# Kernel tuning notes

Measured on AMD Instinct MI355X. Metric: run time of the kernel, lower is better.

The kernel has to match this reference:

```python
import jax, jax.numpy as jnp
import numpy as np

NUM_USERS = 4096
NUM_ITEMS = 4096
NUM_CLASSES = 5
INPUT_DIM = 64
H0 = 64   # hidden[0]
H1 = 32   # hidden[1]
BU = 2048
BV = 2048


def setup_inputs() -> dict:
    key = jax.random.key(0)
    ks = jax.random.split(key, 9)
    ridx = jax.random.randint(ks[0], (NUM_USERS, NUM_ITEMS), 0, NUM_CLASSES * 10)
    ratings = (jnp.arange(NUM_CLASSES)[:, None, None] == ridx[None]).astype(jnp.float32)
    u = jax.random.randint(ks[1], (BU,), 0, NUM_USERS)
    v = jax.random.randint(ks[2], (BV,), 0, NUM_ITEMS)
    u_emb = jax.random.normal(ks[3], (NUM_USERS, INPUT_DIM), jnp.float32) * 0.1
    v_emb = jax.random.normal(ks[4], (NUM_ITEMS, INPUT_DIM), jnp.float32) * 0.1
    gc_w = jax.random.normal(ks[5], (NUM_CLASSES, INPUT_DIM, H0), jnp.float32) / np.sqrt(INPUT_DIM)
    gc_b = jnp.zeros((NUM_CLASSES, H0), jnp.float32)
    dense_w = jax.random.normal(ks[6], (H0, H1), jnp.float32) / np.sqrt(H0)
    dense_b = jnp.zeros((H1,), jnp.float32)
    dec_w = jax.random.normal(ks[7], (NUM_CLASSES, H1, H1), jnp.float32) / np.sqrt(H1)
    return dict(u=u, v=v, ratings=ratings, u_emb=u_emb, v_emb=v_emb,
                gc_w=gc_w, gc_b=gc_b, dense_w=dense_w, dense_b=dense_b, dec_w=dec_w)


def reference(u, v, ratings, u_emb, v_emb, gc_w, gc_b, dense_w, dense_b, dec_w):
    bu = u.shape[0]
    # m = index_select(index_select(ratings, 1, u), 2, v)  -> [C, bu, bv]
    m = ratings[:, u][:, :, v]
    ue = u_emb[u]                      # [bu, D]
    ve = v_emb[v]                      # [bv, D]
    # Degree normalization exactly as in the torch code:
    # du = |sum over dim1 then dim0| -> per-item counts [bv]; di -> per-user counts [bu]
    du = jnp.abs(jnp.sum(m, axis=(0, 1)))
    di = jnp.abs(jnp.sum(m, axis=(0, 2)))
    c = jnp.concatenate([du, di])      # [bv + bu] (requires bu == bv, as in original)
    c = jnp.where(c > 0, 1.0 / c, 0.0)
    x = jnp.concatenate([ue, ve], axis=0)              # [bu+bv, D]
    # Per-class graph convolution, summed over rating classes.
    support = jnp.einsum('nd,cdh->cnh', x, gc_w)       # [C, N, H0]
    su, sv = support[:, :bu], support[:, bu:]
    agg_u = jnp.einsum('cuv,cvh->cuh', m, sv)          # users aggregate items
    agg_v = jnp.einsum('cuv,cuh->cvh', m, su)          # items aggregate users
    agg = jnp.concatenate([agg_u, agg_v], axis=1)      # [C, N, H0]
    z = jnp.sum(c[None, :, None] * agg + gc_b[:, None, :], axis=0)
    z = jax.nn.relu(z)
    hidden = jax.nn.sigmoid(z @ dense_w + dense_b)     # [N, H1]
    hu, hv = hidden[:bu], hidden[bu:]
    # Bilinear decoder: per-class logits u^T W_c v  -> [C, bu, bv]
    logits = jnp.einsum('ud,cde,ve->cuv', hu, dec_w, hv)
    probs = jax.nn.softmax(logits, axis=0)
    classes = jnp.arange(NUM_CLASSES, dtype=hidden.dtype)
    m_hat = jnp.einsum('c,cuv->uv', classes, probs)    # expected rating
    observed = jnp.sum(m, axis=0)                      # [bu, bv] in {0,1}
    n_obs = jnp.maximum(jnp.sum(observed), 1.0)
    logp = jax.nn.log_softmax(logits, axis=0)
    loss = -jnp.sum(m * logp) / n_obs
    pred = jnp.argmax(logits, axis=0)
    true = jnp.argmax(m, axis=0)
    accuracy = jnp.sum((pred == true) * observed) / n_obs
    return m_hat, loss, accuracy
```

## Files before the change

kernel.cpp:

```cpp
#include <hip/hip_runtime.h>
#include <hip/hip_bf16.h>
#include <cstdint>

#define RST 16777216
typedef unsigned short u16;
typedef unsigned char u8;
typedef unsigned int u32;
typedef __attribute__((ext_vector_type(8))) short short8v;
typedef __attribute__((ext_vector_type(4))) float f32x4;

__device__ __forceinline__ u16 f2bf(float x){
  unsigned int b = __float_as_uint(x);
  unsigned int r = (b + 0x7FFFu + ((b >> 16) & 1u)) >> 16;
  return (u16)r;
}
__device__ __forceinline__ float bf2f(u16 h){
  return __uint_as_float(((unsigned int)h) << 16);
}
__device__ __forceinline__ void split8(const float* fa, short8v& hi, short8v& lo){
#pragma unroll
  for (int e = 0; e < 8; e++){
    u16 h = f2bf(fa[e]);
    hi[e] = (short)h;
    lo[e] = (short)f2bf(fa[e] - bf2f(h));
  }
}
__device__ __forceinline__ int cnt_not5(u32 w){
  int c = 0;
  c += ((w & 255u) != 5u); c += (((w >> 8) & 255u) != 5u);
  c += (((w >> 16) & 255u) != 5u); c += ((w >> 24) != 5u);
  return c;
}

__global__ __launch_bounds__(256) void k_labels(const int* __restrict__ u, const int* __restrict__ v,
                                                const float* __restrict__ ratings, u8* __restrict__ L,
                                                int* __restrict__ di){
  __shared__ float row[4096];
  __shared__ int wsum[4];
  int i = blockIdx.x;
  int tid = threadIdx.x;
  int lane = tid & 63, wid = tid >> 6;
  int U = u[i];
  int j0 = tid * 8;
  int vj[8];
#pragma unroll
  for (int k = 0; k < 8; k++) vj[k] = v[j0 + k];
  int lab[8];
#pragma unroll
  for (int k = 0; k < 8; k++) lab[k] = 5;
  const float* rbase = ratings + (size_t)U * 4096;
  for (int c = 0; c < 5; c++){
    const float4* src = (const float4*)(rbase + (size_t)c * RST);
#pragma unroll
    for (int k = 0; k < 4; k++) ((float4*)row)[tid + k*256] = src[tid + k*256];
    __syncthreads();
#pragma unroll
    for (int k = 0; k < 8; k++) if (row[vj[k]] > 0.5f) lab[k] = c;
    __syncthreads();
  }
  unsigned int lo = 0, hi = 0;
  int cnt = 0;
#pragma unroll
  for (int k = 0; k < 4; k++){
    lo |= ((unsigned)lab[k]) << (8*k); hi |= ((unsigned)lab[k+4]) << (8*k);
    cnt += (lab[k] != 5); cnt += (lab[k+4] != 5);
  }
  *(uint2*)(L + (size_t)i * 2048 + j0) = make_uint2(lo, hi);
#pragma unroll
  for (int o = 32; o > 0; o >>= 1) cnt += __shfl_down(cnt, o);
  if (lane == 0) wsum[wid] = cnt;
  __syncthreads();
  if (tid == 0) di[i] = wsum[0] + wsum[1] + wsum[2] + wsum[3];
}

__global__ __launch_bounds__(256) void k_trsup(const u8* __restrict__ L, u8* __restrict__ LT,
    const int* __restrict__ u, const int* __restrict__ v,
    const float* __restrict__ u_emb, const float* __restrict__ v_emb, const float* __restrict__ gc_w,
    u32* __restrict__ SP){
  __shared__ u8 tile[64][64];
  int tid = threadIdx.x;
  if (blockIdx.x < 1024){
    int jb = blockIdx.x & 31, ib = blockIdx.x >> 5;
    int i0 = ib * 64, j0 = jb * 64;
    int r = tid >> 2, cq = tid & 3;
    uint4 d = *(const uint4*)(L + (size_t)(i0 + r) * 2048 + j0 + cq * 16);
    *(uint4*)&tile[r][cq * 16] = d;
    __syncthreads();
    u8 ob[16];
#pragma unroll
    for (int k = 0; k < 16; k++) ob[k] = tile[cq * 16 + k][r];
    *(uint4*)(LT + (size_t)(j0 + r) * 2048 + i0 + cq * 16) = *(uint4*)ob;
  } else {
    int b = blockIdx.x - 1024;
    int c = b >> 6, nblk = b & 63;
    int lane = tid & 63, wv = tid >> 6;
    int m = lane & 15, q = lane >> 4;
    int n0 = nblk * 64;
    bool uside = (n0 < 2048);
    const int* nidx = uside ? u : v;
    const float* emb = uside ? u_emb : v_emb;
    int nbase = uside ? n0 : (n0 - 2048);
    int h0 = wv * 16;
    short8v bh[2], bl[2];
#pragma unroll
    for (int ch = 0; ch < 2; ch++){
      const float* wp = gc_w + c * 4096 + (ch * 32 + q * 8) * 64 + h0 + m;
      float fb[8];
#pragma unroll
      for (int e = 0; e < 8; e++) fb[e] = wp[e * 64];
      split8(fb, bh[ch], bl[ch]);
    }
#pragma unroll
    for (int rt = 0; rt < 4; rt++){
      const float* xr = emb + (size_t)nidx[nbase + rt * 16 + m] * 64;
      f32x4 acc = {0.f, 0.f, 0.f, 0.f};
#pragma unroll
      for (int ch = 0; ch < 2; ch++){
        float fa[8];
        *(float4*)&fa[0] = *(const float4*)(xr + ch * 32 + q * 8);
        *(float4*)&fa[4] = *(const float4*)(xr + ch * 32 + q * 8 + 4);
        short8v ah, al;
        split8(fa, ah, al);
        acc = __builtin_amdgcn_mfma_f32_16x16x32_bf16(ah, bh[ch], acc, 0, 0, 0);
        acc = __builtin_amdgcn_mfma_f32_16x16x32_bf16(ah, bl[ch], acc, 0, 0, 0);
        acc = __builtin_amdgcn_mfma_f32_16x16x32_bf16(al, bh[ch], acc, 0, 0, 0);
      }
      int h = h0 + m;
      int rbase = n0 + rt * 16 + q * 4;
#pragma unroll
      for (int reg = 0; reg < 4; reg++){
        float val = acc[reg];
        u16 vh = f2bf(val);
        u16 vl = f2bf(val - bf2f(vh));
        SP[(((size_t)c * 64 + h) << 12) + rbase + reg] = (((u32)vh) << 16) | (u32)vl;
      }
    }
  }
}

__global__ __launch_bounds__(256) void k_agg(const u8* __restrict__ L, const u8* __restrict__ LT,
    const u32* __restrict__ SP, float* __restrict__ aggp){
  int tid = threadIdx.x;
  int lane = tid & 63, wv = tid >> 6;
  int m = lane & 15, q = lane >> 4;
  int kc = blockIdx.x;
  int rb = blockIdx.y;
  int r0 = rb * 64;
  bool uside = (r0 < 2048);
  const u8* Ab = uside ? (L + (size_t)r0 * 2048) : (LT + (size_t)(r0 - 2048) * 2048);
  int nb = uside ? 2048 : 0;
  int h0 = wv * 16;
  f32x4 acc[4];
#pragma unroll
  for (int it = 0; it < 4; it++) acc[it] = (f32x4){0.f, 0.f, 0.f, 0.f};
  for (int ks = 0; ks < 4; ks++){
    int j0 = (kc * 4 + ks) * 32;
    short8v bh[5], bl[5];
#pragma unroll
    for (int c = 0; c < 5; c++){
      const uint4* bp = (const uint4*)(SP + (((size_t)c * 64 + h0 + m) << 12) + nb + j0 + q * 8);
      uint4 wA = bp[0], wB = bp[1];
      u32 wws[8] = {wA.x, wA.y, wA.z, wA.w, wB.x, wB.y, wB.z, wB.w};
#pragma unroll
      for (int e = 0; e < 8; e++){
        bh[c][e] = (short)(wws[e] >> 16);
        bl[c][e] = (short)(wws[e] & 0xffffu);
      }
    }
#pragma unroll
    for (int it = 0; it < 4; it++){
      uint2 aw = *(const uint2*)(Ab + (size_t)(it * 16 + m) * 2048 + j0 + q * 8);
      int b[8];
#pragma unroll
      for (int e = 0; e < 4; e++){ b[e] = (aw.x >> (8*e)) & 255; b[e+4] = (aw.y >> (8*e)) & 255; }
#pragma unroll
      for (int c = 0; c < 5; c++){
        short8v am;
#pragma unroll
        for (int e = 0; e < 8; e++) am[e] = (short)((b[e] == c) ? 0x3F80 : 0);
        acc[it] = __builtin_amdgcn_mfma_f32_16x16x32_bf16(am, bh[c], acc[it], 0, 0, 0);
        acc[it] = __builtin_amdgcn_mfma_f32_16x16x32_bf16(am, bl[c], acc[it], 0, 0, 0);
      }
    }
  }
  float* op = aggp + (size_t)kc * 262144;
#pragma unroll
  for (int it = 0; it < 4; it++){
#pragma unroll
    for (int reg = 0; reg < 4; reg++)
      op[(size_t)(r0 + it * 16 + q * 4 + reg) * 64 + h0 + m] = acc[it][reg];
  }
}

__global__ __launch_bounds__(256) void k_hidden(const float* __restrict__ aggp, const u8* __restrict__ LT,
    const int* __restrict__ di,
    const float* __restrict__ gc_b, const float* __restrict__ dense_w, const float* __restrict__ dense_b,
    float* __restrict__ hidden){
  int wid = threadIdx.x >> 6, lane = threadIdx.x & 63;
  int r = blockIdx.x * 4 + wid;
  float a = 0.f;
#pragma unroll
  for (int kc = 0; kc < 16; kc++) a += aggp[(size_t)kc * 262144 + (size_t)r * 64 + lane];
  int cnt;
  if (r < 2048){
    const uint4* rp = (const uint4*)(LT + (size_t)r * 2048);
    uint4 w1 = rp[lane * 2], w2 = rp[lane * 2 + 1];
    int c2 = cnt_not5(w1.x) + cnt_not5(w1.y) + cnt_not5(w1.z) + cnt_not5(w1.w)
           + cnt_not5(w2.x) + cnt_not5(w2.y) + cnt_not5(w2.z) + cnt_not5(w2.w);
#pragma unroll
    for (int o = 32; o > 0; o >>= 1) c2 += __shfl_down(c2, o);
    cnt = __shfl(c2, 0);
  } else {
    cnt = di[r - 2048];
  }
  float inv = (cnt > 0) ? (1.0f / (float)cnt) : 0.0f;
  float bsum = 0.f;
#pragma unroll
  for (int c = 0; c < 5; c++) bsum += gc_b[c * 64 + lane];
  float z = fmaxf(a * inv + bsum, 0.f);
  __shared__ float zb[4][64];
  zb[wid][lane] = z;
  __syncthreads();
  if (lane < 32){
    float s = dense_b[lane];
#pragma unroll
    for (int h = 0; h < 64; h++) s += zb[wid][h] * dense_w[h * 32 + lane];
    hidden[(size_t)r * 32 + lane] = 1.0f / (1.0f + __expf(-s));
  }
}

#define EPI(l, lab, outp) do{ \
  float mx = fmaxf(fmaxf(fmaxf(l[0], l[1]), fmaxf(l[2], l[3])), l[4]); \
  float e0 = __expf(l[0]-mx), e1 = __expf(l[1]-mx), e2 = __expf(l[2]-mx), e3 = __expf(l[3]-mx), e4 = __expf(l[4]-mx); \
  float ssum = e0 + e1 + e2 + e3 + e4; \
  *(outp) = (e1 + 2.f*e2 + 3.f*e3 + 4.f*e4) / ssum; \
  if ((lab) < 5){ \
    int pred = 0; float bm = l[0]; \
    if (l[1] > bm){ bm = l[1]; pred = 1; } \
    if (l[2] > bm){ bm = l[2]; pred = 2; } \
    if (l[3] > bm){ bm = l[3]; pred = 3; } \
    if (l[4] > bm){ bm = l[4]; pred = 4; } \
    float ll = (lab)==0 ? l[0] : ((lab)==1 ? l[1] : ((lab)==2 ? l[2] : ((lab)==3 ? l[3] : l[4]))); \
    lsum += __logf(ssum) + mx - ll; \
    acnt += (pred == (lab)); \
  } \
}while(0)

__global__ __launch_bounds__(256) void k_logits(const float* __restrict__ hidden, const float* __restrict__ dec_w,
    const u8* __restrict__ L, float* __restrict__ mhat, float* __restrict__ lpart, int* __restrict__ apart){
  __shared__ float hu_s[512];
  __shared__ float tsf[5 * 16 * 36];
  int tid = threadIdx.x;
  int lane = tid & 63, w = tid >> 6;
  int i0 = blockIdx.y * 16;
  if (tid < 128) ((float4*)hu_s)[tid] = ((const float4*)(hidden + (size_t)i0 * 32))[tid];
  __syncthreads();
  for (int idx = tid; idx < 2560; idx += 256){
    int c = idx >> 9; int rem = idx & 511; int ii = rem >> 5; int e = rem & 31;
    const float* wc = dec_w + (size_t)c * 1024 + e;
    const float* hr = hu_s + ii * 32;
    float s = 0.f;
#pragma unroll
    for (int d = 0; d < 32; d++) s += hr[d] * wc[d * 32];
    tsf[(c * 16 + ii) * 36 + e] = s;
  }
  __syncthreads();
  int m = lane & 15, q = lane >> 4;
  short8v a_hi[5], a_lo[5];
#pragma unroll
  for (int c = 0; c < 5; c++){
    const float* p = &tsf[(c * 16 + m) * 36 + q * 8];
    float fa[8];
    *(float4*)&fa[0] = *(const float4*)p;
    *(float4*)&fa[4] = *(const float4*)(p + 4);
    split8(fa, a_hi[c], a_lo[c]);
  }
  const float* hv = hidden + 2048 * 32;
  float lsum = 0.f; int acnt = 0;
  int jw0 = blockIdx.x * 256 + w * 64;
#pragma unroll
  for (int jj = 0; jj < 4; jj++){
    int j0 = jw0 + jj * 16;
    const float* pb = hv + (size_t)(j0 + m) * 32 + q * 8;
    float fb[8];
    *(float4*)&fb[0] = *(const float4*)pb;
    *(float4*)&fb[4] = *(const float4*)(pb + 4);
    short8v b_hi, b_lo;
    split8(fb, b_hi, b_lo);
    f32x4 acc[5];
    f32x4 z4 = {0.f, 0.f, 0.f, 0.f};
#pragma unroll
    for (int c = 0; c < 5; c++){
      f32x4 a = __builtin_amdgcn_mfma_f32_16x16x32_bf16(a_hi[c], b_hi, z4, 0, 0, 0);
      a = __builtin_amdgcn_mfma_f32_16x16x32_bf16(a_hi[c], b_lo, a, 0, 0, 0);
      a = __builtin_amdgcn_mfma_f32_16x16x32_bf16(a_lo[c], b_hi, a, 0, 0, 0);
      acc[c] = a;
    }
    int jcol = j0 + m;
#pragma unroll
    for (int r = 0; r < 4; r++){
      int irow = i0 + q * 4 + r;
      float l5[5] = {acc[0][r], acc[1][r], acc[2][r], acc[3][r], acc[4][r]};
      int lab = L[(size_t)irow * 2048 + jcol];
      EPI(l5, lab, mhat + (size_t)irow * 2048 + jcol);
    }
  }
#pragma unroll
  for (int o = 32; o > 0; o >>= 1){ lsum += __shfl_down(lsum, o); acnt += __shfl_down(acnt, o); }
  __shared__ float wl[4]; __shared__ int wa[4];
  if (lane == 0){ wl[w] = lsum; wa[w] = acnt; }
  __syncthreads();
  if (tid == 0){
    int pb = blockIdx.y * 8 + blockIdx.x;
    lpart[pb] = wl[0] + wl[1] + wl[2] + wl[3];
    apart[pb] = wa[0] + wa[1] + wa[2] + wa[3];
  }
}

__global__ __launch_bounds__(256) void k_final(const float* __restrict__ lpart, const int* __restrict__ apart,
                                               const int* __restrict__ di, float* __restrict__ out){
  __shared__ float lred[256];
  __shared__ int ared[256], nred[256];
  int tid = threadIdx.x;
  float ls = 0.f; int as = 0;
#pragma unroll
  for (int k = 0; k < 4; k++){ ls += lpart[tid + k * 256]; as += apart[tid + k * 256]; }
  int ns = 0;
#pragma unroll
  for (int k = 0; k < 8; k++) ns += di[tid + k * 256];
  lred[tid] = ls; ared[tid] = as; nred[tid] = ns;
  __syncthreads();
  for (int s = 128; s > 0; s >>= 1){
    if (tid < s){ lred[tid] += lred[tid + s]; ared[tid] += ared[tid + s]; nred[tid] += nred[tid + s]; }
    __syncthreads();
  }
  if (tid == 0){
    float n = fmaxf((float)nred[0], 1.0f);
    out[0] = lred[0] / n;
    out[1] = ((float)ared[0]) / n;
  }
}

extern "C" void kernel_launch(void* const* d_in, const int* in_sizes, int n_in,
                              void* d_out, int out_size, void* d_ws, size_t ws_size,
                              hipStream_t stream){
  const int*   u       = (const int*)d_in[0];
  const int*   v       = (const int*)d_in[1];
  const float* ratings = (const float*)d_in[2];
  const float* u_emb   = (const float*)d_in[3];
  const float* v_emb   = (const float*)d_in[4];
  const float* gc_w    = (const float*)d_in[5];
  const float* gc_b    = (const float*)d_in[6];
  const float* dense_w = (const float*)d_in[7];
  const float* dense_b = (const float*)d_in[8];
  const float* dec_w   = (const float*)d_in[9];
  float* out = (float*)d_out;
  char* ws = (char*)d_ws;

  u8*    L       = (u8*)(ws + 0);
  u8*    LT      = (u8*)(ws + 4194304);
  u32*   SP      = (u32*)(ws + 8388608);
  float* aggp    = (float*)(ws + 13631488);
  float* hidden  = (float*)(ws + 30408704);
  int*   di      = (int*)(ws + 30932992);
  float* lpart   = (float*)(ws + 30941184);
  int*   apart   = (int*)(ws + 30945280);

  k_labels <<<2048, 256, 0, stream>>>(u, v, ratings, L, di);
  k_trsup  <<<1344, 256, 0, stream>>>(L, LT, u, v, u_emb, v_emb, gc_w, SP);
  k_agg    <<<dim3(16, 64), 256, 0, stream>>>(L, LT, SP, aggp);
  k_hidden <<<1024, 256, 0, stream>>>(aggp, LT, di, gc_b, dense_w, dense_b, hidden);
  k_logits <<<dim3(8, 128), 256, 0, stream>>>(hidden, dec_w, L, out, lpart, apart);
  k_final  <<<1, 256, 0, stream>>>(lpart, apart, di, out + 4194304);
}
```

Baseline: 104.4 us.

## Pre-pack support into MFMA fragment layout and stage label tiles in LDS

The support matrix is now written by k_trsup in a fragment-ordered layout, so each lane in k_agg reads its B operand as contiguous 32-byte chunks. k_agg stages its 64x256 label tile in shared memory and halves the k-split from 16 to 8 chunks, doubling the per-block K loop. This cuts the aggp partials that k_hidden must sum and shrinks the workspace. The cost is fewer blocks in k_agg (512) and an extra LDS staging pass with a barrier in k_trsup.

After: 94.57 us. -9.4%, faster.

```diff
diff --git a/kernel.cpp b/kernel.cpp
--- a/kernel.cpp
+++ b/kernel.cpp
@@ -6,6 +6,7 @@
 typedef unsigned short u16;
 typedef unsigned char u8;
 typedef unsigned int u32;
+typedef unsigned long long u64;
 typedef __attribute__((ext_vector_type(8))) short short8v;
 typedef __attribute__((ext_vector_type(4))) float f32x4;
 
@@ -76,19 +77,19 @@
 __global__ __launch_bounds__(256) void k_trsup(const u8* __restrict__ L, u8* __restrict__ LT,
     const int* __restrict__ u, const int* __restrict__ v,
     const float* __restrict__ u_emb, const float* __restrict__ v_emb, const float* __restrict__ gc_w,
-    u32* __restrict__ SP){
-  __shared__ u8 tile[64][64];
+    u32* __restrict__ SPF){
+  __shared__ union { u8 tile[64][64]; u32 pack[4096]; } sm;
   int tid = threadIdx.x;
   if (blockIdx.x < 1024){
     int jb = blockIdx.x & 31, ib = blockIdx.x >> 5;
     int i0 = ib * 64, j0 = jb * 64;
     int r = tid >> 2, cq = tid & 3;
     uint4 d = *(const uint4*)(L + (size_t)(i0 + r) * 2048 + j0 + cq * 16);
-    *(uint4*)&tile[r][cq * 16] = d;
+    *(uint4*)&sm.tile[r][cq * 16] = d;
     __syncthreads();
     u8 ob[16];
 #pragma unroll
-    for (int k = 0; k < 16; k++) ob[k] = tile[cq * 16 + k][r];
+    for (int k = 0; k < 16; k++) ob[k] = sm.tile[cq * 16 + k][r];
     *(uint4*)(LT + (size_t)(j0 + r) * 2048 + i0 + cq * 16) = *(uint4*)ob;
   } else {
     int b = blockIdx.x - 1024;
@@ -125,21 +126,33 @@
         acc = __builtin_amdgcn_mfma_f32_16x16x32_bf16(ah, bl[ch], acc, 0, 0, 0);
         acc = __builtin_amdgcn_mfma_f32_16x16x32_bf16(al, bh[ch], acc, 0, 0, 0);
       }
-      int h = h0 + m;
-      int rbase = n0 + rt * 16 + q * 4;
 #pragma unroll
       for (int reg = 0; reg < 4; reg++){
         float val = acc[reg];
         u16 vh = f2bf(val);
         u16 vl = f2bf(val - bf2f(vh));
-        SP[(((size_t)c * 64 + h) << 12) + rbase + reg] = (((u32)vh) << 16) | (u32)vl;
+        int n = n0 + rt * 16 + q * 4 + reg;
+        int jc_l = (n >> 5) & 1;
+        int kk = n & 31;
+        int lanep = m + ((kk >> 3) << 4);
+        int ep = kk & 7;
+        sm.pack[((jc_l * 4 + wv) * 64 + lanep) * 8 + ep] = (((u32)vh) << 16) | (u32)vl;
       }
     }
+    __syncthreads();
+    int jc0 = n0 >> 5;
+    u32* dst = SPF + ((size_t)(c * 128 + jc0) * 4) * 512;
+#pragma unroll
+    for (int p = 0; p < 4; p++){
+      int t = p * 1024 + tid * 4;
+      *(uint4*)&dst[t] = *(const uint4*)&sm.pack[t];
+    }
   }
 }
 
 __global__ __launch_bounds__(256) void k_agg(const u8* __restrict__ L, const u8* __restrict__ LT,
-    const u32* __restrict__ SP, float* __restrict__ aggp){
+    const u32* __restrict__ SPF, float* __restrict__ aggp){
+  __shared__ u8 As[64][272];
   int tid = threadIdx.x;
   int lane = tid & 63, wv = tid >> 6;
   int m = lane & 15, q = lane >> 4;
@@ -148,17 +161,22 @@
   int r0 = rb * 64;
   bool uside = (r0 < 2048);
   const u8* Ab = uside ? (L + (size_t)r0 * 2048) : (LT + (size_t)(r0 - 2048) * 2048);
-  int nb = uside ? 2048 : 0;
-  int h0 = wv * 16;
+  int jcb = (uside ? 64 : 0) + kc * 8;
+#pragma unroll
+  for (int p = 0; p < 4; p++){
+    int idx = p * 256 + tid;
+    int row = idx >> 4, ci = idx & 15;
+    *(uint4*)&As[row][ci * 16] = *(const uint4*)(Ab + (size_t)row * 2048 + kc * 256 + ci * 16);
+  }
+  __syncthreads();
   f32x4 acc[4];
 #pragma unroll
   for (int it = 0; it < 4; it++) acc[it] = (f32x4){0.f, 0.f, 0.f, 0.f};
-  for (int ks = 0; ks < 4; ks++){
-    int j0 = (kc * 4 + ks) * 32;
+  for (int ks = 0; ks < 8; ks++){
     short8v bh[5], bl[5];
 #pragma unroll
     for (int c = 0; c < 5; c++){
-      const uint4* bp = (const uint4*)(SP + (((size_t)c * 64 + h0 + m) << 12) + nb + j0 + q * 8);
+      const uint4* bp = (const uint4*)(SPF + ((size_t)((c * 128 + jcb + ks) * 4 + wv) * 64 + lane) * 8);
       uint4 wA = bp[0], wB = bp[1];
       u32 wws[8] = {wA.x, wA.y, wA.z, wA.w, wB.x, wB.y, wB.z, wB.w};
 #pragma unroll
@@ -169,10 +187,10 @@
     }
 #pragma unroll
     for (int it = 0; it < 4; it++){
-      uint2 aw = *(const uint2*)(Ab + (size_t)(it * 16 + m) * 2048 + j0 + q * 8);
+      u64 a8 = *(const u64*)&As[it * 16 + m][ks * 32 + q * 8];
       int b[8];
 #pragma unroll
-      for (int e = 0; e < 4; e++){ b[e] = (aw.x >> (8*e)) & 255; b[e+4] = (aw.y >> (8*e)) & 255; }
+      for (int e = 0; e < 8; e++) b[e] = (int)((a8 >> (8 * e)) & 255u);
 #pragma unroll
       for (int c = 0; c < 5; c++){
         short8v am;
@@ -184,6 +202,7 @@
     }
   }
   float* op = aggp + (size_t)kc * 262144;
+  int h0 = wv * 16;
 #pragma unroll
   for (int it = 0; it < 4; it++){
 #pragma unroll
@@ -200,7 +219,7 @@
   int r = blockIdx.x * 4 + wid;
   float a = 0.f;
 #pragma unroll
-  for (int kc = 0; kc < 16; kc++) a += aggp[(size_t)kc * 262144 + (size_t)r * 64 + lane];
+  for (int kc = 0; kc < 8; kc++) a += aggp[(size_t)kc * 262144 + (size_t)r * 64 + lane];
   int cnt;
   if (r < 2048){
     const uint4* rp = (const uint4*)(LT + (size_t)r * 2048);
@@ -359,16 +378,16 @@
 
   u8*    L       = (u8*)(ws + 0);
   u8*    LT      = (u8*)(ws + 4194304);
-  u32*   SP      = (u32*)(ws + 8388608);
+  u32*   SPF     = (u32*)(ws + 8388608);
   float* aggp    = (float*)(ws + 13631488);
-  float* hidden  = (float*)(ws + 30408704);
-  int*   di      = (int*)(ws + 30932992);
-  float* lpart   = (float*)(ws + 30941184);
-  int*   apart   = (int*)(ws + 30945280);
+  float* hidden  = (float*)(ws + 22020096);
+  int*   di      = (int*)(ws + 22544384);
+  float* lpart   = (float*)(ws + 22552576);
+  int*   apart   = (int*)(ws + 22556672);
 
   k_labels <<<2048, 256, 0, stream>>>(u, v, ratings, L, di);
-  k_trsup  <<<1344, 256, 0, stream>>>(L, LT, u, v, u_emb, v_emb, gc_w, SP);
-  k_agg    <<<dim3(16, 64), 256, 0, stream>>>(L, LT, SP, aggp);
+  k_trsup  <<<1344, 256, 0, stream>>>(L, LT, u, v, u_emb, v_emb, gc_w, SPF);
+  k_agg    <<<dim3(8, 64), 256, 0, stream>>>(L, LT, SPF, aggp);
   k_hidden <<<1024, 256, 0, stream>>>(aggp, LT, di, gc_b, dense_w, dense_b, hidden);
   k_logits <<<dim3(8, 128), 256, 0, stream>>>(hidden, dec_w, L, out, lpart, apart);
   k_final  <<<1, 256, 0, stream>>>(lpart, apart, di, out + 4194304);
```
